# Kernel optimization log

Measured on AMD Instinct MI355X. Metric: run time of the kernel, lower is better.

## Reference

```python
import jax, jax.numpy as jnp
import numpy as np

B, T_MEL, T_TXT = 16, 2048, 1024
D_MODEL, D_ENC_M, D_ENC_T = 512, 512, 512
LN_EPS = 1e-5


def setup_inputs() -> dict:
    key = jax.random.key(0)
    ks = jax.random.split(key, 9)
    mel_encoding = jax.random.normal(ks[0], (B, T_MEL, D_ENC_M), dtype=jnp.float32)
    text_encoding = jax.random.normal(ks[1], (B, T_TXT, D_ENC_T), dtype=jnp.float32)
    mel_mask = jax.random.randint(ks[2], (B, T_MEL), 0, 2).astype(bool)
    mel_mask = mel_mask.at[:, 0].set(False)  # guarantee >=1 unmasked key per row
    src_mask = jax.random.randint(ks[3], (B, T_TXT), 0, 2).astype(bool)
    # Projection weights stored [in, out] (torch Linear does x @ W.T)
    sc = 1.0 / np.sqrt(D_ENC_M)
    Wq = jax.random.uniform(ks[4], (D_ENC_T, D_MODEL), jnp.float32, -sc, sc)
    Wk = jax.random.uniform(ks[5], (D_ENC_M, D_MODEL), jnp.float32, -sc, sc)
    Wv = jax.random.uniform(ks[6], (D_ENC_M, D_MODEL), jnp.float32, -sc, sc)
    ln_gamma = jnp.ones((D_MODEL,), jnp.float32)
    ln_beta = jnp.zeros((D_MODEL,), jnp.float32)
    return {"mel_encoding": mel_encoding, "text_encoding": text_encoding,
            "mel_mask": mel_mask, "src_mask": src_mask,
            "Wq": Wq, "Wk": Wk, "Wv": Wv,
            "ln_gamma": ln_gamma, "ln_beta": ln_beta}


def reference(mel_encoding, text_encoding, mel_mask, src_mask, Wq, Wk, Wv, ln_gamma, ln_beta):
    temperature = jnp.sqrt(jnp.float32(D_ENC_M))
    q = jnp.einsum('btd,dm->btm', text_encoding, Wq)   # [B, T_txt, d_model]
    k = jnp.einsum('bsd,dm->bsm', mel_encoding, Wk)    # [B, T_mel, d_model]
    v = jnp.einsum('bsd,dm->bsm', mel_encoding, Wv)
    # attn_mask = outer product of src_mask and mel_mask (True -> masked)
    attn_mask = src_mask[:, :, None] & mel_mask[:, None, :]  # [B, T_txt, T_mel]
    scores = jnp.einsum('btm,bsm->bts', q, k) / temperature
    scores = jnp.where(attn_mask, -jnp.inf, scores)
    attn = jax.nn.softmax(scores, axis=2)
    output = jnp.einsum('bts,bsm->btm', attn, v)
    # dropout is identity at inference; LayerNorm over last dim
    mean = jnp.mean(output, axis=-1, keepdims=True)
    var = jnp.var(output, axis=-1, keepdims=True)
    output = (output - mean) * jax.lax.rsqrt(var + LN_EPS) * ln_gamma + ln_beta
    return output, attn
```

## Files before the change

kernel.cpp:

```cpp
#include <hip/hip_runtime.h>

#define DEV __device__ __forceinline__

typedef __attribute__((ext_vector_type(8))) short short8v;
typedef __attribute__((ext_vector_type(4))) float f32x4;

DEV unsigned short f2bf(float f) {
  unsigned int x = __float_as_uint(f);
  x = x + 0x7FFFu + ((x >> 16) & 1u);
  return (unsigned short)(x >> 16);
}

DEV int swz_byte(int row, int kElem) {
  int chunk = ((kElem >> 3) ^ (row & 7));
  return row * 128 + (chunk << 4) + ((kElem & 7) << 1);
}

template <int ROUNDS>
DEV void stage(const unsigned short* __restrict__ g, int ld,
               unsigned short* tile, int tid) {
  const int wave = tid >> 6, l = tid & 63;
#pragma unroll
  for (int p = 0; p < ROUNDS; ++p) {
    const int r = (p << 5) + (wave << 3) + (l >> 3);
    const int c = ((l & 7) ^ (r & 7)) << 3;
    const unsigned short* src = g + (long)r * ld + c;
#if __has_builtin(__builtin_amdgcn_global_load_lds)
    unsigned short* dst = tile + (p << 11) + (wave << 9);
    __builtin_amdgcn_global_load_lds(
        (const __attribute__((address_space(1))) void*)src,
        (__attribute__((address_space(3))) void*)dst, 16, 0, 0);
#else
    short8v v = *reinterpret_cast<const short8v*>(src);
    *reinterpret_cast<short8v*>(reinterpret_cast<char*>(tile) +
                                (p << 12) + (wave << 10) + (l << 4)) = v;
#endif
  }
}

template <int BM, int EPI>
__global__ __launch_bounds__(256) void gemm_bf16(
    const unsigned short* __restrict__ A, const unsigned short* __restrict__ B,
    void* __restrict__ Cout, int M, int N, int K,
    long aBatch, long bBatch, long cBatch,
    const int* __restrict__ srcMask, const int* __restrict__ melMask,
    float scale) {
  constexpr int NI = BM / 32;
  __shared__ unsigned short As[BM * 64];
  __shared__ unsigned short Bs[128 * 64];
  const int tid = threadIdx.x;
  const int lane = tid & 63;
  const int wave = tid >> 6;
  const int z = blockIdx.z;
  const unsigned short* Ab = A + (long)z * aBatch;
  const unsigned short* Bb = B + (long)z * bBatch;
  const long cOff = (long)z * cBatch;
  const int bm = blockIdx.y * BM;
  const int bn = blockIdx.x * 128;
  const int wr = (wave >> 1) * (BM / 2);
  const int wc = (wave & 1) * 64;
  const int l15 = lane & 15;
  const int lHi = lane >> 4;

  f32x4 acc[NI][4] = {};

  for (int kt = 0; kt < K; kt += 64) {
    stage<BM / 32>(Ab + (long)bm * K + kt, K, As, tid);
    stage<4>(Bb + (long)bn * K + kt, K, Bs, tid);
    __syncthreads();
#pragma unroll
    for (int ks = 0; ks < 2; ++ks) {
      const int k0 = (ks << 5) + (lHi << 3);
      short8v af[NI], bfr[4];
#pragma unroll
      for (int i = 0; i < NI; ++i)
        af[i] = *reinterpret_cast<const short8v*>(
            reinterpret_cast<const char*>(As) + swz_byte(wr + i * 16 + l15, k0));
#pragma unroll
      for (int j = 0; j < 4; ++j)
        bfr[j] = *reinterpret_cast<const short8v*>(
            reinterpret_cast<const char*>(Bs) + swz_byte(wc + j * 16 + l15, k0));
#pragma unroll
      for (int i = 0; i < NI; ++i)
#pragma unroll
        for (int j = 0; j < 4; ++j)
          acc[i][j] = __builtin_amdgcn_mfma_f32_16x16x32_bf16(af[i], bfr[j], acc[i][j], 0, 0, 0);
    }
    __syncthreads();
  }

#pragma unroll
  for (int i = 0; i < NI; ++i) {
#pragma unroll
    for (int j = 0; j < 4; ++j) {
      const int rb = bm + wr + i * 16 + lHi * 4;
      const int c = bn + wc + j * 16 + l15;
#pragma unroll
      for (int r = 0; r < 4; ++r) {
        const float v = acc[i][j][r];
        const long idx = cOff + (long)(rb + r) * N + c;
        if constexpr (EPI == 0) {
          reinterpret_cast<unsigned short*>(Cout)[idx] = f2bf(v);
        } else if constexpr (EPI == 1) {
          reinterpret_cast<float*>(Cout)[idx] = v;
        } else {
          const bool sm = srcMask[z * 1024 + (rb + r)] != 0;
          const bool mm = melMask[z * 2048 + c] != 0;
          reinterpret_cast<float*>(Cout)[idx] = (sm && mm) ? -1e30f : v * scale;
        }
      }
    }
  }
}

__global__ __launch_bounds__(256) void f32_to_bf16(
    const float* __restrict__ in, unsigned short* __restrict__ out, long n) {
  long i = ((long)blockIdx.x * blockDim.x + threadIdx.x) * 8;
  const long stride = (long)gridDim.x * blockDim.x * 8;
  for (; i < n; i += stride) {
    const float4 a = *reinterpret_cast<const float4*>(in + i);
    const float4 b = *reinterpret_cast<const float4*>(in + i + 4);
    short8v o;
    o[0] = (short)f2bf(a.x); o[1] = (short)f2bf(a.y);
    o[2] = (short)f2bf(a.z); o[3] = (short)f2bf(a.w);
    o[4] = (short)f2bf(b.x); o[5] = (short)f2bf(b.y);
    o[6] = (short)f2bf(b.z); o[7] = (short)f2bf(b.w);
    *reinterpret_cast<short8v*>(out + i) = o;
  }
}

__global__ __launch_bounds__(256) void transpose_w3(
    const float* __restrict__ Wq, const float* __restrict__ Wk, const float* __restrict__ Wv,
    unsigned short* __restrict__ WqT, unsigned short* __restrict__ WkT,
    unsigned short* __restrict__ WvT) {
  __shared__ float t[32][33];
  const int zz = blockIdx.z;
  const float* W = zz == 0 ? Wq : zz == 1 ? Wk : Wv;
  unsigned short* WT = zz == 0 ? WqT : zz == 1 ? WkT : WvT;
  const int bx = blockIdx.x * 32;
  const int by = blockIdx.y * 32;
  const int tx = threadIdx.x, ty = threadIdx.y;
#pragma unroll
  for (int i = 0; i < 4; ++i)
    t[ty + i * 8][tx] = W[(long)(by + ty + i * 8) * 512 + bx + tx];
  __syncthreads();
#pragma unroll
  for (int i = 0; i < 4; ++i)
    WT[(long)(bx + ty + i * 8) * 512 + by + tx] = f2bf(t[tx][ty + i * 8]);
}

__global__ __launch_bounds__(256) void softmax_rows(
    float* __restrict__ attn, unsigned short* __restrict__ pbf) {
  const long row = blockIdx.x;
  float4* p = reinterpret_cast<float4*>(attn + row * 2048);
  const int tid = threadIdx.x;
  float4 a = p[tid];
  float4 b = p[tid + 256];
  float m = fmaxf(fmaxf(fmaxf(a.x, a.y), fmaxf(a.z, a.w)),
                  fmaxf(fmaxf(b.x, b.y), fmaxf(b.z, b.w)));
#pragma unroll
  for (int o = 32; o; o >>= 1) m = fmaxf(m, __shfl_xor(m, o, 64));
  __shared__ float redm[4];
  if ((tid & 63) == 0) redm[tid >> 6] = m;
  __syncthreads();
  m = fmaxf(fmaxf(redm[0], redm[1]), fmaxf(redm[2], redm[3]));
  float e0 = __expf(a.x - m), e1 = __expf(a.y - m), e2 = __expf(a.z - m), e3 = __expf(a.w - m);
  float e4 = __expf(b.x - m), e5 = __expf(b.y - m), e6 = __expf(b.z - m), e7 = __expf(b.w - m);
  float s = ((e0 + e1) + (e2 + e3)) + ((e4 + e5) + (e6 + e7));
#pragma unroll
  for (int o = 32; o; o >>= 1) s += __shfl_xor(s, o, 64);
  __shared__ float reds[4];
  if ((tid & 63) == 0) reds[tid >> 6] = s;
  __syncthreads();
  s = (reds[0] + reds[1]) + (reds[2] + reds[3]);
  const float inv = 1.0f / s;
  a.x = e0 * inv; a.y = e1 * inv; a.z = e2 * inv; a.w = e3 * inv;
  b.x = e4 * inv; b.y = e5 * inv; b.z = e6 * inv; b.w = e7 * inv;
  p[tid] = a;
  p[tid + 256] = b;
  ushort4 o0, o1;
  o0.x = f2bf(a.x); o0.y = f2bf(a.y); o0.z = f2bf(a.z); o0.w = f2bf(a.w);
  o1.x = f2bf(b.x); o1.y = f2bf(b.y); o1.z = f2bf(b.z); o1.w = f2bf(b.w);
  *reinterpret_cast<ushort4*>(pbf + row * 2048 + tid * 4) = o0;
  *reinterpret_cast<ushort4*>(pbf + row * 2048 + 1024 + tid * 4) = o1;
}

__global__ __launch_bounds__(64) void layernorm_rows(
    float* __restrict__ out, const float* __restrict__ gamma, const float* __restrict__ beta) {
  const long row = blockIdx.x;
  float4* p = reinterpret_cast<float4*>(out + row * 512);
  const int lane = threadIdx.x;
  float4 a = p[lane];
  float4 b = p[lane + 64];
  float s = ((a.x + a.y) + (a.z + a.w)) + ((b.x + b.y) + (b.z + b.w));
  float s2 = ((a.x * a.x + a.y * a.y) + (a.z * a.z + a.w * a.w)) +
             ((b.x * b.x + b.y * b.y) + (b.z * b.z + b.w * b.w));
#pragma unroll
  for (int o = 32; o; o >>= 1) {
    s += __shfl_xor(s, o, 64);
    s2 += __shfl_xor(s2, o, 64);
  }
  const float mean = s * (1.0f / 512.0f);
  const float var = s2 * (1.0f / 512.0f) - mean * mean;
  const float rstd = rsqrtf(var + 1e-5f);
  const float4 g0 = reinterpret_cast<const float4*>(gamma)[lane];
  const float4 g1 = reinterpret_cast<const float4*>(gamma)[lane + 64];
  const float4 c0 = reinterpret_cast<const float4*>(beta)[lane];
  const float4 c1 = reinterpret_cast<const float4*>(beta)[lane + 64];
  a.x = (a.x - mean) * rstd * g0.x + c0.x;
  a.y = (a.y - mean) * rstd * g0.y + c0.y;
  a.z = (a.z - mean) * rstd * g0.z + c0.z;
  a.w = (a.w - mean) * rstd * g0.w + c0.w;
  b.x = (b.x - mean) * rstd * g1.x + c1.x;
  b.y = (b.y - mean) * rstd * g1.y + c1.y;
  b.z = (b.z - mean) * rstd * g1.z + c1.z;
  b.w = (b.w - mean) * rstd * g1.w + c1.w;
  p[lane] = a;
  p[lane + 64] = b;
}

extern "C" void kernel_launch(void* const* d_in, const int* in_sizes, int n_in,
                              void* d_out, int out_size, void* d_ws, size_t ws_size,
                              hipStream_t stream) {
  const float* mel  = (const float*)d_in[0];
  const float* text = (const float*)d_in[1];
  const int* melMask = (const int*)d_in[2];
  const int* srcMask = (const int*)d_in[3];
  const float* Wq = (const float*)d_in[4];
  const float* Wk = (const float*)d_in[5];
  const float* Wv = (const float*)d_in[6];
  const float* gamma = (const float*)d_in[7];
  const float* beta  = (const float*)d_in[8];

  float* out = (float*)d_out;
  float* attn = (float*)d_out + (long)16 * 1024 * 512;

  unsigned short* ws = (unsigned short*)d_ws;
  unsigned short* wqT = ws;
  unsigned short* wkT = wqT + 512 * 512;
  unsigned short* wvT = wkT + 512 * 512;
  unsigned short* melbf  = wvT + 512 * 512;
  unsigned short* textbf = melbf + (long)16 * 2048 * 512;
  unsigned short* qbf = textbf + (long)16 * 1024 * 512;
  unsigned short* kbf = qbf + (long)16 * 1024 * 512;
  unsigned short* vT  = kbf + (long)16 * 2048 * 512;
  unsigned short* pbf = melbf;

  transpose_w3<<<dim3(16, 16, 3), dim3(32, 8), 0, stream>>>(Wq, Wk, Wv, wqT, wkT, wvT);
  f32_to_bf16<<<dim3(4096), 256, 0, stream>>>(mel, melbf, (long)16 * 2048 * 512);
  f32_to_bf16<<<dim3(2048), 256, 0, stream>>>(text, textbf, (long)16 * 1024 * 512);

  gemm_bf16<128, 0><<<dim3(4, 128, 1), 256, 0, stream>>>(
      textbf, wqT, qbf, 16384, 512, 512, 0, 0, 0, nullptr, nullptr, 1.0f);
  gemm_bf16<128, 0><<<dim3(4, 256, 1), 256, 0, stream>>>(
      melbf, wkT, kbf, 32768, 512, 512, 0, 0, 0, nullptr, nullptr, 1.0f);
  gemm_bf16<128, 0><<<dim3(16, 4, 16), 256, 0, stream>>>(
      wvT, melbf, vT, 512, 2048, 512, 0, (long)2048 * 512, (long)512 * 2048,
      nullptr, nullptr, 1.0f);
  gemm_bf16<128, 2><<<dim3(16, 8, 16), 256, 0, stream>>>(
      qbf, kbf, attn, 1024, 2048, 512,
      (long)1024 * 512, (long)2048 * 512, (long)1024 * 2048,
      srcMask, melMask, 0.044194173824159216f);
  softmax_rows<<<dim3(16 * 1024), 256, 0, stream>>>(attn, pbf);
  gemm_bf16<64, 1><<<dim3(4, 16, 16), 256, 0, stream>>>(
      pbf, vT, out, 1024, 512, 2048,
      (long)1024 * 2048, (long)512 * 2048, (long)1024 * 512,
      nullptr, nullptr, 1.0f);
  layernorm_rows<<<dim3(16 * 1024), 64, 0, stream>>>(out, gamma, beta);
}
```

Baseline: 309.5 us.

## Fuse softmax stats into QK epilogue and normalize inside PV GEMM

The score GEMM epilogue now computes a per-tile row max and sum-of-exponentials and writes them to a small stats buffer placed where textbf used to be. A new softmax_pv kernel merges these partial stats, normalizes the scores while loading them, writes the final attn, converts to bf16 in LDS, and runs the PV matmul with a 64x512 output tile. This removes the separate softmax pass over the 128MB score matrix and the bf16 P round trip. The cost is a grid of only 256 blocks of 512 threads with a large LDS footprint, so occupancy and latency hiding are lower.

After: 324.9 us. 1.05x slower.

```diff
diff --git a/kernel.cpp b/kernel.cpp
--- a/kernel.cpp
+++ b/kernel.cpp
@@ -44,7 +44,7 @@
     void* __restrict__ Cout, int M, int N, int K,
     long aBatch, long bBatch, long cBatch,
     const int* __restrict__ srcMask, const int* __restrict__ melMask,
-    float scale) {
+    float scale, float* __restrict__ stats) {
   constexpr int NI = BM / 32;
   __shared__ unsigned short As[BM * 64];
   __shared__ unsigned short Bs[128 * 64];
@@ -89,28 +89,170 @@
     __syncthreads();
   }
 
-#pragma unroll
-  for (int i = 0; i < NI; ++i) {
-#pragma unroll
-    for (int j = 0; j < 4; ++j) {
-      const int rb = bm + wr + i * 16 + lHi * 4;
-      const int c = bn + wc + j * 16 + l15;
-#pragma unroll
-      for (int r = 0; r < 4; ++r) {
-        const float v = acc[i][j][r];
-        const long idx = cOff + (long)(rb + r) * N + c;
-        if constexpr (EPI == 0) {
-          reinterpret_cast<unsigned short*>(Cout)[idx] = f2bf(v);
-        } else if constexpr (EPI == 1) {
-          reinterpret_cast<float*>(Cout)[idx] = v;
-        } else {
-          const bool sm = srcMask[z * 1024 + (rb + r)] != 0;
+  if constexpr (EPI == 2) {
+    __shared__ float redM[128][2];
+    __shared__ float redS[128][2];
+    const int wcIdx = wave & 1;
+#pragma unroll
+    for (int i = 0; i < NI; ++i) {
+#pragma unroll
+      for (int rr = 0; rr < 4; ++rr) {
+        const int rloc = wr + i * 16 + lHi * 4 + rr;
+        const int rb = bm + rloc;
+        const bool sm = srcMask[z * 1024 + rb] != 0;
+        float vals[4];
+        float m_l = -3.0e38f;
+#pragma unroll
+        for (int j = 0; j < 4; ++j) {
+          const int c = bn + wc + j * 16 + l15;
           const bool mm = melMask[z * 2048 + c] != 0;
-          reinterpret_cast<float*>(Cout)[idx] = (sm && mm) ? -1e30f : v * scale;
+          const float vf = (sm && mm) ? -1e30f : acc[i][j][rr] * scale;
+          vals[j] = vf;
+          reinterpret_cast<float*>(Cout)[cOff + (long)rb * N + c] = vf;
+          m_l = fmaxf(m_l, vf);
+        }
+#pragma unroll
+        for (int o = 1; o < 16; o <<= 1) m_l = fmaxf(m_l, __shfl_xor(m_l, o, 64));
+        float s_l = 0.f;
+#pragma unroll
+        for (int j = 0; j < 4; ++j) s_l += __expf(vals[j] - m_l);
+#pragma unroll
+        for (int o = 1; o < 16; o <<= 1) s_l += __shfl_xor(s_l, o, 64);
+        if (l15 == 0) { redM[rloc][wcIdx] = m_l; redS[rloc][wcIdx] = s_l; }
+      }
+    }
+    __syncthreads();
+    if (tid < 128) {
+      const float m0 = redM[tid][0], m1 = redM[tid][1];
+      const float Mx = fmaxf(m0, m1);
+      const float S = redS[tid][0] * __expf(m0 - Mx) + redS[tid][1] * __expf(m1 - Mx);
+      const long sidx = ((long)(z * 1024 + bm + tid)) * 32 + (long)blockIdx.x * 2;
+      stats[sidx] = Mx;
+      stats[sidx + 1] = S;
+    }
+  } else {
+#pragma unroll
+    for (int i = 0; i < NI; ++i) {
+#pragma unroll
+      for (int j = 0; j < 4; ++j) {
+        const int rb = bm + wr + i * 16 + lHi * 4;
+        const int c = bn + wc + j * 16 + l15;
+#pragma unroll
+        for (int r = 0; r < 4; ++r) {
+          const float v = acc[i][j][r];
+          const long idx = cOff + (long)(rb + r) * N + c;
+          if constexpr (EPI == 0)
+            reinterpret_cast<unsigned short*>(Cout)[idx] = f2bf(v);
+          else
+            reinterpret_cast<float*>(Cout)[idx] = v;
         }
       }
     }
   }
+}
+
+__global__ __launch_bounds__(512) void softmax_pv(
+    float* __restrict__ attn, const unsigned short* __restrict__ vT,
+    float* __restrict__ out, const float* __restrict__ stats) {
+  __shared__ unsigned short As[64 * 64];
+  __shared__ unsigned short Bs[512 * 64];
+  __shared__ float rowM[64], rowInv[64];
+  const int z = blockIdx.x;
+  const int bm = blockIdx.y * 64;
+  const int tid = threadIdx.x, lane = tid & 63, wave = tid >> 6;
+  const long sOff = ((long)z * 1024 + bm) * 2048;
+
+  if (tid < 64) {
+    const float* st = stats + ((long)(z * 1024 + bm + tid)) * 32;
+    float Mx = -3.0e38f;
+#pragma unroll
+    for (int t = 0; t < 16; ++t) Mx = fmaxf(Mx, st[t * 2]);
+    float S = 0.f;
+#pragma unroll
+    for (int t = 0; t < 16; ++t) S += st[t * 2 + 1] * __expf(st[t * 2] - Mx);
+    rowM[tid] = Mx;
+    rowInv[tid] = 1.0f / S;
+  }
+  __syncthreads();
+
+  const int r = tid >> 3;
+  const int c8 = (tid & 7) << 3;
+  const float mR = rowM[r];
+  const float invR = rowInv[r];
+  const int wr2 = (wave >> 2) * 32;
+  const int wc2 = (wave & 3) * 128;
+  const int l15 = lane & 15, lHi = lane >> 4;
+
+  f32x4 acc[2][8] = {};
+
+  for (int kt = 0; kt < 2048; kt += 64) {
+    {
+      float* sp = attn + sOff + (long)r * 2048 + kt + c8;
+      const float4 x0 = *reinterpret_cast<const float4*>(sp);
+      const float4 x1 = *reinterpret_cast<const float4*>(sp + 4);
+      float4 e0, e1;
+      e0.x = __expf(x0.x - mR) * invR; e0.y = __expf(x0.y - mR) * invR;
+      e0.z = __expf(x0.z - mR) * invR; e0.w = __expf(x0.w - mR) * invR;
+      e1.x = __expf(x1.x - mR) * invR; e1.y = __expf(x1.y - mR) * invR;
+      e1.z = __expf(x1.z - mR) * invR; e1.w = __expf(x1.w - mR) * invR;
+      *reinterpret_cast<float4*>(sp) = e0;
+      *reinterpret_cast<float4*>(sp + 4) = e1;
+      short8v pk;
+      pk[0] = (short)f2bf(e0.x); pk[1] = (short)f2bf(e0.y);
+      pk[2] = (short)f2bf(e0.z); pk[3] = (short)f2bf(e0.w);
+      pk[4] = (short)f2bf(e1.x); pk[5] = (short)f2bf(e1.y);
+      pk[6] = (short)f2bf(e1.z); pk[7] = (short)f2bf(e1.w);
+      *reinterpret_cast<short8v*>(reinterpret_cast<char*>(As) + r * 128 +
+                                  ((((tid & 7) ^ (r & 7))) << 4)) = pk;
+    }
+#pragma unroll
+    for (int p = 0; p < 8; ++p) {
+      const int r2 = (p << 6) + (wave << 3) + (lane >> 3);
+      const int cc = ((lane & 7) ^ (r2 & 7)) << 3;
+      const unsigned short* srcB = vT + (long)z * 512 * 2048 + (long)r2 * 2048 + kt + cc;
+#if __has_builtin(__builtin_amdgcn_global_load_lds)
+      unsigned short* dst = Bs + ((p << 6) + (wave << 3)) * 64;
+      __builtin_amdgcn_global_load_lds(
+          (const __attribute__((address_space(1))) void*)srcB,
+          (__attribute__((address_space(3))) void*)dst, 16, 0, 0);
+#else
+      short8v v = *reinterpret_cast<const short8v*>(srcB);
+      *reinterpret_cast<short8v*>(reinterpret_cast<char*>(Bs) +
+                                  ((p << 6) + (wave << 3)) * 128 + (lane << 4)) = v;
+#endif
+    }
+    __syncthreads();
+#pragma unroll
+    for (int ks = 0; ks < 2; ++ks) {
+      const int k0 = (ks << 5) + (lHi << 3);
+      short8v af[2], bfr[8];
+#pragma unroll
+      for (int i = 0; i < 2; ++i)
+        af[i] = *reinterpret_cast<const short8v*>(
+            reinterpret_cast<const char*>(As) + swz_byte(wr2 + i * 16 + l15, k0));
+#pragma unroll
+      for (int j = 0; j < 8; ++j)
+        bfr[j] = *reinterpret_cast<const short8v*>(
+            reinterpret_cast<const char*>(Bs) + swz_byte(wc2 + j * 16 + l15, k0));
+#pragma unroll
+      for (int i = 0; i < 2; ++i)
+#pragma unroll
+        for (int j = 0; j < 8; ++j)
+          acc[i][j] = __builtin_amdgcn_mfma_f32_16x16x32_bf16(af[i], bfr[j], acc[i][j], 0, 0, 0);
+    }
+    __syncthreads();
+  }
+
+#pragma unroll
+  for (int i = 0; i < 2; ++i)
+#pragma unroll
+    for (int j = 0; j < 8; ++j) {
+      const int row = bm + wr2 + i * 16 + lHi * 4;
+      const int col = wc2 + j * 16 + l15;
+#pragma unroll
+      for (int rr = 0; rr < 4; ++rr)
+        out[((long)z * 1024 + row + rr) * 512 + col] = acc[i][j][rr];
+    }
 }
 
 __global__ __launch_bounds__(256) void f32_to_bf16(
@@ -147,42 +289,6 @@
 #pragma unroll
   for (int i = 0; i < 4; ++i)
     WT[(long)(bx + ty + i * 8) * 512 + by + tx] = f2bf(t[tx][ty + i * 8]);
-}
-
-__global__ __launch_bounds__(256) void softmax_rows(
-    float* __restrict__ attn, unsigned short* __restrict__ pbf) {
-  const long row = blockIdx.x;
-  float4* p = reinterpret_cast<float4*>(attn + row * 2048);
-  const int tid = threadIdx.x;
-  float4 a = p[tid];
-  float4 b = p[tid + 256];
-  float m = fmaxf(fmaxf(fmaxf(a.x, a.y), fmaxf(a.z, a.w)),
-                  fmaxf(fmaxf(b.x, b.y), fmaxf(b.z, b.w)));
-#pragma unroll
-  for (int o = 32; o; o >>= 1) m = fmaxf(m, __shfl_xor(m, o, 64));
-  __shared__ float redm[4];
-  if ((tid & 63) == 0) redm[tid >> 6] = m;
-  __syncthreads();
-  m = fmaxf(fmaxf(redm[0], redm[1]), fmaxf(redm[2], redm[3]));
-  float e0 = __expf(a.x - m), e1 = __expf(a.y - m), e2 = __expf(a.z - m), e3 = __expf(a.w - m);
-  float e4 = __expf(b.x - m), e5 = __expf(b.y - m), e6 = __expf(b.z - m), e7 = __expf(b.w - m);
-  float s = ((e0 + e1) + (e2 + e3)) + ((e4 + e5) + (e6 + e7));
-#pragma unroll
-  for (int o = 32; o; o >>= 1) s += __shfl_xor(s, o, 64);
-  __shared__ float reds[4];
-  if ((tid & 63) == 0) reds[tid >> 6] = s;
-  __syncthreads();
-  s = (reds[0] + reds[1]) + (reds[2] + reds[3]);
-  const float inv = 1.0f / s;
-  a.x = e0 * inv; a.y = e1 * inv; a.z = e2 * inv; a.w = e3 * inv;
-  b.x = e4 * inv; b.y = e5 * inv; b.z = e6 * inv; b.w = e7 * inv;
-  p[tid] = a;
-  p[tid + 256] = b;
-  ushort4 o0, o1;
-  o0.x = f2bf(a.x); o0.y = f2bf(a.y); o0.z = f2bf(a.z); o0.w = f2bf(a.w);
-  o1.x = f2bf(b.x); o1.y = f2bf(b.y); o1.z = f2bf(b.z); o1.w = f2bf(b.w);
-  *reinterpret_cast<ushort4*>(pbf + row * 2048 + tid * 4) = o0;
-  *reinterpret_cast<ushort4*>(pbf + row * 2048 + 1024 + tid * 4) = o1;
 }
 
 __global__ __launch_bounds__(64) void layernorm_rows(
@@ -244,27 +350,23 @@
   unsigned short* qbf = textbf + (long)16 * 1024 * 512;
   unsigned short* kbf = qbf + (long)16 * 1024 * 512;
   unsigned short* vT  = kbf + (long)16 * 2048 * 512;
-  unsigned short* pbf = melbf;
+  float* stats = (float*)textbf;
 
   transpose_w3<<<dim3(16, 16, 3), dim3(32, 8), 0, stream>>>(Wq, Wk, Wv, wqT, wkT, wvT);
   f32_to_bf16<<<dim3(4096), 256, 0, stream>>>(mel, melbf, (long)16 * 2048 * 512);
   f32_to_bf16<<<dim3(2048), 256, 0, stream>>>(text, textbf, (long)16 * 1024 * 512);
 
   gemm_bf16<128, 0><<<dim3(4, 128, 1), 256, 0, stream>>>(
-      textbf, wqT, qbf, 16384, 512, 512, 0, 0, 0, nullptr, nullptr, 1.0f);
+      textbf, wqT, qbf, 16384, 512, 512, 0, 0, 0, nullptr, nullptr, 1.0f, nullptr);
   gemm_bf16<128, 0><<<dim3(4, 256, 1), 256, 0, stream>>>(
-      melbf, wkT, kbf, 32768, 512, 512, 0, 0, 0, nullptr, nullptr, 1.0f);
+      melbf, wkT, kbf, 32768, 512, 512, 0, 0, 0, nullptr, nullptr, 1.0f, nullptr);
   gemm_bf16<128, 0><<<dim3(16, 4, 16), 256, 0, stream>>>(
       wvT, melbf, vT, 512, 2048, 512, 0, (long)2048 * 512, (long)512 * 2048,
-      nullptr, nullptr, 1.0f);
+      nullptr, nullptr, 1.0f, nullptr);
   gemm_bf16<128, 2><<<dim3(16, 8, 16), 256, 0, stream>>>(
       qbf, kbf, attn, 1024, 2048, 512,
       (long)1024 * 512, (long)2048 * 512, (long)1024 * 2048,
-      srcMask, melMask, 0.044194173824159216f);
-  softmax_rows<<<dim3(16 * 1024), 256, 0, stream>>>(attn, pbf);
-  gemm_bf16<64, 1><<<dim3(4, 16, 16), 256, 0, stream>>>(
-      pbf, vT, out, 1024, 512, 2048,
-      (long)1024 * 2048, (long)512 * 2048, (long)1024 * 512,
-      nullptr, nullptr, 1.0f);
+      srcMask, melMask, 0.044194173824159216f, stats);
+  softmax_pv<<<dim3(16, 16), 512, 0, stream>>>(attn, vT, out, stats);
   layernorm_rows<<<dim3(16 * 1024), 64, 0, stream>>>(out, gamma, beta);
 }
```

## Fuse softmax statistics into QK GEMM epilogue and store bf16 scores

Applied to the files above, without the earlier changes.

The score GEMM epilogue now writes masked, scaled scores as bf16 and computes per-tile row max and exp-sums. It reduces them across the two column waves and writes them to a stats buffer. A new finalize kernel combines the 16 partial stats per row, reads the bf16 scores once, and writes both the fp32 attention output and the bf16 probabilities for the PV GEMM. This removes the fp32 score write and re-read of the separate softmax pass, at the cost of rounding scores to bf16 before the exponential and needing a larger workspace; a fallback keeps the old path when the workspace is too small.

Measured after the change: 312.7 us. About the same (+1.0%).

```diff
diff --git a/kernel.cpp b/kernel.cpp
--- a/kernel.cpp
+++ b/kernel.cpp
@@ -44,7 +44,7 @@
     void* __restrict__ Cout, int M, int N, int K,
     long aBatch, long bBatch, long cBatch,
     const int* __restrict__ srcMask, const int* __restrict__ melMask,
-    float scale) {
+    float scale, float* __restrict__ stats) {
   constexpr int NI = BM / 32;
   __shared__ unsigned short As[BM * 64];
   __shared__ unsigned short Bs[128 * 64];
@@ -89,64 +89,106 @@
     __syncthreads();
   }
 
-#pragma unroll
-  for (int i = 0; i < NI; ++i) {
-#pragma unroll
-    for (int j = 0; j < 4; ++j) {
-      const int rb = bm + wr + i * 16 + lHi * 4;
-      const int c = bn + wc + j * 16 + l15;
-#pragma unroll
-      for (int r = 0; r < 4; ++r) {
-        const float v = acc[i][j][r];
-        const long idx = cOff + (long)(rb + r) * N + c;
-        if constexpr (EPI == 0) {
-          reinterpret_cast<unsigned short*>(Cout)[idx] = f2bf(v);
-        } else if constexpr (EPI == 1) {
-          reinterpret_cast<float*>(Cout)[idx] = v;
-        } else {
-          const bool sm = srcMask[z * 1024 + (rb + r)] != 0;
+  if constexpr (EPI >= 2) {
+    __shared__ float redM[128][2];
+    __shared__ float redS[128][2];
+    const int wcIdx = wave & 1;
+#pragma unroll
+    for (int i = 0; i < NI; ++i) {
+#pragma unroll
+      for (int rr = 0; rr < 4; ++rr) {
+        const int rloc = wr + i * 16 + lHi * 4 + rr;
+        const int rb = bm + rloc;
+        const bool sm = srcMask[z * 1024 + rb] != 0;
+        float vals[4];
+        float m_l = -3.0e38f;
+#pragma unroll
+        for (int j = 0; j < 4; ++j) {
+          const int c = bn + wc + j * 16 + l15;
           const bool mm = melMask[z * 2048 + c] != 0;
-          reinterpret_cast<float*>(Cout)[idx] = (sm && mm) ? -1e30f : v * scale;
+          const float vf = (sm && mm) ? -1e30f : acc[i][j][rr] * scale;
+          vals[j] = vf;
+          if constexpr (EPI == 2)
+            reinterpret_cast<unsigned short*>(Cout)[cOff + (long)rb * N + c] = f2bf(vf);
+          else
+            reinterpret_cast<float*>(Cout)[cOff + (long)rb * N + c] = vf;
+          m_l = fmaxf(m_l, vf);
+        }
+        if (stats) {
+#pragma unroll
+          for (int o = 1; o < 16; o <<= 1) m_l = fmaxf(m_l, __shfl_xor(m_l, o, 64));
+          float s_l = 0.f;
+#pragma unroll
+          for (int j = 0; j < 4; ++j) s_l += __expf(vals[j] - m_l);
+#pragma unroll
+          for (int o = 1; o < 16; o <<= 1) s_l += __shfl_xor(s_l, o, 64);
+          if (l15 == 0) { redM[rloc][wcIdx] = m_l; redS[rloc][wcIdx] = s_l; }
         }
       }
     }
-  }
-}
-
-__global__ __launch_bounds__(256) void f32_to_bf16(
-    const float* __restrict__ in, unsigned short* __restrict__ out, long n) {
-  long i = ((long)blockIdx.x * blockDim.x + threadIdx.x) * 8;
-  const long stride = (long)gridDim.x * blockDim.x * 8;
-  for (; i < n; i += stride) {
-    const float4 a = *reinterpret_cast<const float4*>(in + i);
-    const float4 b = *reinterpret_cast<const float4*>(in + i + 4);
-    short8v o;
-    o[0] = (short)f2bf(a.x); o[1] = (short)f2bf(a.y);
-    o[2] = (short)f2bf(a.z); o[3] = (short)f2bf(a.w);
-    o[4] = (short)f2bf(b.x); o[5] = (short)f2bf(b.y);
-    o[6] = (short)f2bf(b.z); o[7] = (short)f2bf(b.w);
-    *reinterpret_cast<short8v*>(out + i) = o;
-  }
-}
-
-__global__ __launch_bounds__(256) void transpose_w3(
-    const float* __restrict__ Wq, const float* __restrict__ Wk, const float* __restrict__ Wv,
-    unsigned short* __restrict__ WqT, unsigned short* __restrict__ WkT,
-    unsigned short* __restrict__ WvT) {
-  __shared__ float t[32][33];
-  const int zz = blockIdx.z;
-  const float* W = zz == 0 ? Wq : zz == 1 ? Wk : Wv;
-  unsigned short* WT = zz == 0 ? WqT : zz == 1 ? WkT : WvT;
-  const int bx = blockIdx.x * 32;
-  const int by = blockIdx.y * 32;
-  const int tx = threadIdx.x, ty = threadIdx.y;
-#pragma unroll
-  for (int i = 0; i < 4; ++i)
-    t[ty + i * 8][tx] = W[(long)(by + ty + i * 8) * 512 + bx + tx];
-  __syncthreads();
-#pragma unroll
-  for (int i = 0; i < 4; ++i)
-    WT[(long)(bx + ty + i * 8) * 512 + by + tx] = f2bf(t[tx][ty + i * 8]);
+    if (stats) {
+      __syncthreads();
+      if (tid < 128) {
+        const float m0 = redM[tid][0], m1 = redM[tid][1];
+        const float Mx = fmaxf(m0, m1);
+        const float S = redS[tid][0] * __expf(m0 - Mx) + redS[tid][1] * __expf(m1 - Mx);
+        const long sidx = ((long)(z * 1024 + bm + tid)) * 32 + (long)blockIdx.x * 2;
+        stats[sidx] = Mx;
+        stats[sidx + 1] = S;
+      }
+    }
+  } else {
+#pragma unroll
+    for (int i = 0; i < NI; ++i) {
+#pragma unroll
+      for (int j = 0; j < 4; ++j) {
+        const int rb = bm + wr + i * 16 + lHi * 4;
+        const int c = bn + wc + j * 16 + l15;
+#pragma unroll
+        for (int r = 0; r < 4; ++r) {
+          const float v = acc[i][j][r];
+          const long idx = cOff + (long)(rb + r) * N + c;
+          if constexpr (EPI == 0)
+            reinterpret_cast<unsigned short*>(Cout)[idx] = f2bf(v);
+          else
+            reinterpret_cast<float*>(Cout)[idx] = v;
+        }
+      }
+    }
+  }
+}
+
+__global__ __launch_bounds__(256) void softmax_finalize(
+    unsigned short* __restrict__ sbf, const float* __restrict__ stats,
+    float* __restrict__ attn) {
+  const long row = blockIdx.x;
+  const float* st = stats + row * 32;
+  float Mx = -3.0e38f;
+#pragma unroll
+  for (int t = 0; t < 16; ++t) Mx = fmaxf(Mx, st[t * 2]);
+  float S = 0.f;
+#pragma unroll
+  for (int t = 0; t < 16; ++t) S += st[t * 2 + 1] * __expf(st[t * 2] - Mx);
+  const float inv = 1.0f / S;
+  const int tid = threadIdx.x;
+  unsigned short* sp = sbf + row * 2048 + tid * 8;
+  float* ap = attn + row * 2048 + tid * 8;
+  const short8v sv = *reinterpret_cast<const short8v*>(sp);
+  float e[8];
+#pragma unroll
+  for (int u = 0; u < 8; ++u) {
+    const float s = __uint_as_float(((unsigned)(unsigned short)sv[u]) << 16);
+    e[u] = __expf(s - Mx) * inv;
+  }
+  float4 w0, w1;
+  w0.x = e[0]; w0.y = e[1]; w0.z = e[2]; w0.w = e[3];
+  w1.x = e[4]; w1.y = e[5]; w1.z = e[6]; w1.w = e[7];
+  *reinterpret_cast<float4*>(ap) = w0;
+  *reinterpret_cast<float4*>(ap + 4) = w1;
+  short8v pk;
+#pragma unroll
+  for (int u = 0; u < 8; ++u) pk[u] = (short)f2bf(e[u]);
+  *reinterpret_cast<short8v*>(sp) = pk;
 }
 
 __global__ __launch_bounds__(256) void softmax_rows(
@@ -183,6 +225,42 @@
   o1.x = f2bf(b.x); o1.y = f2bf(b.y); o1.z = f2bf(b.z); o1.w = f2bf(b.w);
   *reinterpret_cast<ushort4*>(pbf + row * 2048 + tid * 4) = o0;
   *reinterpret_cast<ushort4*>(pbf + row * 2048 + 1024 + tid * 4) = o1;
+}
+
+__global__ __launch_bounds__(256) void f32_to_bf16(
+    const float* __restrict__ in, unsigned short* __restrict__ out, long n) {
+  long i = ((long)blockIdx.x * blockDim.x + threadIdx.x) * 8;
+  const long stride = (long)gridDim.x * blockDim.x * 8;
+  for (; i < n; i += stride) {
+    const float4 a = *reinterpret_cast<const float4*>(in + i);
+    const float4 b = *reinterpret_cast<const float4*>(in + i + 4);
+    short8v o;
+    o[0] = (short)f2bf(a.x); o[1] = (short)f2bf(a.y);
+    o[2] = (short)f2bf(a.z); o[3] = (short)f2bf(a.w);
+    o[4] = (short)f2bf(b.x); o[5] = (short)f2bf(b.y);
+    o[6] = (short)f2bf(b.z); o[7] = (short)f2bf(b.w);
+    *reinterpret_cast<short8v*>(out + i) = o;
+  }
+}
+
+__global__ __launch_bounds__(256) void transpose_w3(
+    const float* __restrict__ Wq, const float* __restrict__ Wk, const float* __restrict__ Wv,
+    unsigned short* __restrict__ WqT, unsigned short* __restrict__ WkT,
+    unsigned short* __restrict__ WvT) {
+  __shared__ float t[32][33];
+  const int zz = blockIdx.z;
+  const float* W = zz == 0 ? Wq : zz == 1 ? Wk : Wv;
+  unsigned short* WT = zz == 0 ? WqT : zz == 1 ? WkT : WvT;
+  const int bx = blockIdx.x * 32;
+  const int by = blockIdx.y * 32;
+  const int tx = threadIdx.x, ty = threadIdx.y;
+#pragma unroll
+  for (int i = 0; i < 4; ++i)
+    t[ty + i * 8][tx] = W[(long)(by + ty + i * 8) * 512 + bx + tx];
+  __syncthreads();
+#pragma unroll
+  for (int i = 0; i < 4; ++i)
+    WT[(long)(bx + ty + i * 8) * 512 + by + tx] = f2bf(t[tx][ty + i * 8]);
 }
 
 __global__ __launch_bounds__(64) void layernorm_rows(
@@ -244,27 +322,43 @@
   unsigned short* qbf = textbf + (long)16 * 1024 * 512;
   unsigned short* kbf = qbf + (long)16 * 1024 * 512;
   unsigned short* vT  = kbf + (long)16 * 2048 * 512;
-  unsigned short* pbf = melbf;
+  unsigned short* sbf = vT + (long)16 * 512 * 2048;
+  float* stats = (float*)melbf;
+  const bool bigws = ws_size >= 202899456ull;
 
   transpose_w3<<<dim3(16, 16, 3), dim3(32, 8), 0, stream>>>(Wq, Wk, Wv, wqT, wkT, wvT);
   f32_to_bf16<<<dim3(4096), 256, 0, stream>>>(mel, melbf, (long)16 * 2048 * 512);
   f32_to_bf16<<<dim3(2048), 256, 0, stream>>>(text, textbf, (long)16 * 1024 * 512);
 
   gemm_bf16<128, 0><<<dim3(4, 128, 1), 256, 0, stream>>>(
-      textbf, wqT, qbf, 16384, 512, 512, 0, 0, 0, nullptr, nullptr, 1.0f);
+      textbf, wqT, qbf, 16384, 512, 512, 0, 0, 0, nullptr, nullptr, 1.0f, nullptr);
   gemm_bf16<128, 0><<<dim3(4, 256, 1), 256, 0, stream>>>(
-      melbf, wkT, kbf, 32768, 512, 512, 0, 0, 0, nullptr, nullptr, 1.0f);
+      melbf, wkT, kbf, 32768, 512, 512, 0, 0, 0, nullptr, nullptr, 1.0f, nullptr);
   gemm_bf16<128, 0><<<dim3(16, 4, 16), 256, 0, stream>>>(
       wvT, melbf, vT, 512, 2048, 512, 0, (long)2048 * 512, (long)512 * 2048,
-      nullptr, nullptr, 1.0f);
-  gemm_bf16<128, 2><<<dim3(16, 8, 16), 256, 0, stream>>>(
-      qbf, kbf, attn, 1024, 2048, 512,
-      (long)1024 * 512, (long)2048 * 512, (long)1024 * 2048,
-      srcMask, melMask, 0.044194173824159216f);
-  softmax_rows<<<dim3(16 * 1024), 256, 0, stream>>>(attn, pbf);
-  gemm_bf16<64, 1><<<dim3(4, 16, 16), 256, 0, stream>>>(
-      pbf, vT, out, 1024, 512, 2048,
-      (long)1024 * 2048, (long)512 * 2048, (long)1024 * 512,
-      nullptr, nullptr, 1.0f);
+      nullptr, nullptr, 1.0f, nullptr);
+
+  if (bigws) {
+    gemm_bf16<128, 2><<<dim3(16, 8, 16), 256, 0, stream>>>(
+        qbf, kbf, sbf, 1024, 2048, 512,
+        (long)1024 * 512, (long)2048 * 512, (long)1024 * 2048,
+        srcMask, melMask, 0.044194173824159216f, stats);
+    softmax_finalize<<<dim3(16 * 1024), 256, 0, stream>>>(sbf, stats, attn);
+    gemm_bf16<64, 1><<<dim3(4, 16, 16), 256, 0, stream>>>(
+        sbf, vT, out, 1024, 512, 2048,
+        (long)1024 * 2048, (long)512 * 2048, (long)1024 * 512,
+        nullptr, nullptr, 1.0f, nullptr);
+  } else {
+    unsigned short* pbf = melbf;
+    gemm_bf16<128, 3><<<dim3(16, 8, 16), 256, 0, stream>>>(
+        qbf, kbf, attn, 1024, 2048, 512,
+        (long)1024 * 512, (long)2048 * 512, (long)1024 * 2048,
+        srcMask, melMask, 0.044194173824159216f, nullptr);
+    softmax_rows<<<dim3(16 * 1024), 256, 0, stream>>>(attn, pbf);
+    gemm_bf16<64, 1><<<dim3(4, 16, 16), 256, 0, stream>>>(
+        pbf, vT, out, 1024, 512, 2048,
+        (long)1024 * 2048, (long)512 * 2048, (long)1024 * 512,
+        nullptr, nullptr, 1.0f, nullptr);
+  }
   layernorm_rows<<<dim3(16 * 1024), 64, 0, stream>>>(out, gamma, beta);
 }
```
